# Optimization experiments

Hardware: AMD Instinct MI355X
Metric: run time of the kernel (lower is better)

Reference implementation:

```python
import jax, jax.numpy as jnp
import numpy as np
import math

# dims
B, T, D = 2, 1024, 1024
HQ, HKV, KD, VD = 16, 4, 64, 64   # query heads, kv heads, key dim, value dim
G = HQ // HKV                      # query group size
E, TOPK, CAP_FRAC, HID = 8, 2, 0.5, 2048
BASE = 10000.0
EPS = 1e-6


def setup_inputs() -> dict:
    key = jax.random.key(0)
    ks = jax.random.split(key, 12)
    s = jnp.float32(0.02)
    return {
        'x': jax.random.normal(ks[0], (B, T, D), jnp.float32),
        'wq': jax.random.normal(ks[1], (D, KD * HQ), jnp.float32) * s,
        'wk': jax.random.normal(ks[2], (D, KD * HKV), jnp.float32) * s,
        'wv': jax.random.normal(ks[3], (D, VD * HKV), jnp.float32) * s,
        'wo': jax.random.normal(ks[4], (G * HKV * VD, D), jnp.float32) * s,
        'router_w': jax.random.normal(ks[5], (D, E), jnp.float32) * s,
        'router_b': jax.random.normal(ks[6], (E,), jnp.float32) * s,
        'w1': jax.random.normal(ks[7], (E, D, HID), jnp.float32) * s,
        'w2': jax.random.normal(ks[8], (E, D, HID), jnp.float32) * s,
        'w3': jax.random.normal(ks[9], (E, HID, D), jnp.float32) * s,
        'norm1_scale': jnp.ones((D,), jnp.float32),
        'norm2_scale': jnp.ones((D,), jnp.float32),
    }


def _rms(x, scale):
    return x * jax.lax.rsqrt(jnp.mean(x * x, axis=-1, keepdims=True) + EPS) * scale


def _rope(x):
    # x: (B, t, H, d); rotary per RotaryEmbedding: tile(ticks,(1,2)), neg-half rotation
    t, d = x.shape[1], x.shape[3]
    thetas = BASE ** (-jnp.arange(0, d, 2, dtype=jnp.float32) / d)
    ticks = jnp.outer(jnp.arange(t, dtype=jnp.float32), thetas)
    ticks = jnp.tile(ticks, (1, 2))[None, :, None, :]
    cos, sin = jnp.cos(ticks).astype(x.dtype), jnp.sin(ticks).astype(x.dtype)
    x1, x2 = jnp.split(x, 2, axis=-1)
    neg = jnp.concatenate([-x2, x1], axis=-1)
    return x * cos + neg * sin


def reference(x, wq, wk, wv, wo, router_w, router_b, w1, w2, w3, norm1_scale, norm2_scale):
    b, t, d = x.shape
    # ---- pre-norm grouped-query attention with rotary, causal ----
    h = _rms(x, norm1_scale)
    q = (h @ wq).reshape(b, t, HQ, KD)
    k = (h @ wk).reshape(b, t, HKV, KD)
    v = (h @ wv).reshape(b, t, HKV, VD)
    q = _rope(q)
    k = _rope(k)
    qg = q.reshape(b, t, HKV, G, KD)
    scores = jnp.einsum('bthgk,bshk->bhgts', qg, k) / jnp.sqrt(jnp.asarray(KD, x.dtype))
    causal = jnp.tril(jnp.ones((t, t), bool))
    scores = jnp.where(causal, scores, jnp.asarray(-1e9, scores.dtype))
    probs = jax.nn.softmax(scores, axis=-1)
    attn = jnp.einsum('bhgts,bshv->bthgv', probs, v).reshape(b, t, HQ * VD)
    x = x + attn @ wo
    # ---- pre-norm top-k MoE feed-forward (capacity-masked dispatch/combine) ----
    h2 = _rms(x, norm2_scale)
    xf = h2.reshape(b * t, d)
    logits = xf.astype(jnp.float32) @ router_w + router_b        # router in fp32
    gate, assign = jax.lax.top_k(logits, TOPK)                   # (N,k)
    gate = jax.nn.softmax(gate, axis=-1).astype(x.dtype)
    cap = math.floor(b * t * CAP_FRAC)
    onehot = jax.nn.one_hot(assign, E, dtype=jnp.float32)        # (N,k,E)
    pos = jnp.cumsum(jnp.cumsum(onehot, axis=0), axis=1).astype(jnp.int32)
    mask = onehot * (pos < cap)                                  # capacity mask
    token_mask = jnp.sum(mask, axis=-1)                          # (N,k)
    choices = jnp.sum(jax.nn.one_hot(pos, cap, dtype=jnp.float32) * mask[..., None], axis=1)  # (N,E,cap)
    choices = choices.transpose(1, 2, 0)                         # (E,cap,N)
    exp_idx = jnp.einsum('tke,e->tk', mask, jnp.arange(E, dtype=jnp.float32)).astype(jnp.int32)
    pos_idx = jnp.einsum('tke,tke->tk', mask, pos.astype(jnp.float32)).astype(jnp.int32)
    grouped = jnp.einsum('ect,tD->ecD', choices.astype(x.dtype), xf)  # dispatch: (E,cap,D)
    # gated FF per expert: act(w2(x) * w1(x)) @ w3
    hh = jax.nn.gelu(jnp.einsum('ecd,edh->ech', grouped, w2) * jnp.einsum('ecd,edh->ech', grouped, w1))
    eout = jnp.einsum('ech,ehd->ecd', hh, w3)                    # (E,cap,D)
    gathered = eout[exp_idx, pos_idx].reshape(b, t, TOPK, d)
    tm = token_mask.reshape(b, t, TOPK)
    moe = jnp.where(tm[..., None] != 0, gathered, h2[:, :, None, :])  # dropped tokens fall back to input
    moe = jnp.einsum('btkD,btk->btD', moe, gate.reshape(b, t, TOPK))
    return x + moe
```

## Files before the change

### kernel.cpp

```cpp
#include <hip/hip_runtime.h>
#include <math.h>

#define Dm 1024
#define Tn 1024
#define Bn 2
#define NTOK 2048
#define HQn 16
#define HKVn 4
#define KDn 64
#define VDn 64
#define Gn 4
#define NE 8
#define CAPn 1024
#define HIDn 2048
#define QKVS 1536

using frag_ab = __attribute__((ext_vector_type(8))) short;
using f32x4  = __attribute__((ext_vector_type(4))) float;

__device__ __forceinline__ unsigned short f2bf(float f) {
    union { float f; unsigned int u; } v; v.f = f;
    unsigned int r = v.u + 0x7FFFu + ((v.u >> 16) & 1u);
    return (unsigned short)(r >> 16);
}
__device__ __forceinline__ float bf2f(unsigned short b) {
    union { unsigned int u; float f; } v; v.u = ((unsigned int)b) << 16;
    return v.f;
}
__device__ __forceinline__ float gelu_fast(float y) {
    float z = 0.7978845608028654f * (y + 0.044715f * y * y * y);
    float az = fabsf(z);
    float t = __expf(-2.f * az);
    float th = (1.f - t) / (1.f + t);
    th = copysignf(th, z);
    return 0.5f * y * (1.f + th);
}

#define GLOAD16(gp, lp) __builtin_amdgcn_global_load_lds( \
    (const __attribute__((address_space(1))) void*)(gp), \
    (__attribute__((address_space(3))) void*)(lp), 16, 0, 0)

__global__ void rmsnorm_bf16_kernel(const float* __restrict__ x, const float* __restrict__ scale,
                                    unsigned short* __restrict__ out) {
    int row = blockIdx.x;
    const float* xr = x + (size_t)row * Dm;
    float ss = 0.f;
    for (int d = threadIdx.x; d < Dm; d += 256) { float v = xr[d]; ss += v * v; }
    __shared__ float red[256];
    red[threadIdx.x] = ss; __syncthreads();
    for (int s = 128; s > 0; s >>= 1) {
        if (threadIdx.x < s) red[threadIdx.x] += red[threadIdx.x + s];
        __syncthreads();
    }
    float inv = rsqrtf(red[0] * (1.f / Dm) + 1e-6f);
    for (int d = threadIdx.x; d < Dm; d += 256)
        out[(size_t)row * Dm + d] = f2bf(xr[d] * inv * scale[d]);
}

__global__ void rmsnorm_router_kernel(const float* __restrict__ x2, const float* __restrict__ scale,
                                      const float* __restrict__ rw, const float* __restrict__ rb,
                                      float* __restrict__ h2, int* __restrict__ assign,
                                      float* __restrict__ gate) {
    int row = blockIdx.x;
    const float* xr = x2 + (size_t)row * Dm;
    __shared__ float red[256];
    __shared__ float rowbuf[Dm];
    __shared__ float logits[NE];
    float v4[4]; float ss = 0.f;
    #pragma unroll
    for (int i = 0; i < 4; ++i) { v4[i] = xr[threadIdx.x + 256 * i]; ss += v4[i] * v4[i]; }
    red[threadIdx.x] = ss; __syncthreads();
    for (int s = 128; s > 0; s >>= 1) {
        if (threadIdx.x < s) red[threadIdx.x] += red[threadIdx.x + s];
        __syncthreads();
    }
    float inv = rsqrtf(red[0] * (1.f / Dm) + 1e-6f);
    #pragma unroll
    for (int i = 0; i < 4; ++i) {
        int d = threadIdx.x + 256 * i;
        float h = v4[i] * inv * scale[d];
        h2[(size_t)row * Dm + d] = h;
        rowbuf[d] = h;
    }
    __syncthreads();
    int e = threadIdx.x >> 5, lane32 = threadIdx.x & 31;
    float part = 0.f;
    for (int d = lane32; d < Dm; d += 32) part += rowbuf[d] * rw[(size_t)d * NE + e];
    for (int off = 16; off; off >>= 1) part += __shfl_down(part, off, 32);
    if (lane32 == 0) logits[e] = part + rb[e];
    __syncthreads();
    if (threadIdx.x == 0) {
        int i0 = 0; float m0 = logits[0];
        for (int i = 1; i < NE; ++i) if (logits[i] > m0) { m0 = logits[i]; i0 = i; }
        int i1 = -1; float m1 = -1e30f;
        for (int i = 0; i < NE; ++i) if (i != i0 && logits[i] > m1) { m1 = logits[i]; i1 = i; }
        float e1 = __expf(m1 - m0);
        float s = 1.f + e1;
        assign[row * 2] = i0; assign[row * 2 + 1] = i1;
        gate[row * 2] = 1.f / s; gate[row * 2 + 1] = e1 / s;
    }
}

__global__ void transpose_convert(const float* __restrict__ in, unsigned short* __restrict__ out,
                                  int R, int Cstride, int c_base) {
    int e = blockIdx.z;
    int Cext = gridDim.x * 64;
    in  += (size_t)e * R * Cstride;
    out += (size_t)e * R * Cext;
    __shared__ float T[64][65];
    int tid = threadIdx.x;
    int r0 = blockIdx.y * 64, c0 = blockIdx.x * 64;
    #pragma unroll
    for (int rep = 0; rep < 4; ++rep) {
        int r = (tid >> 4) + rep * 16;
        int c = (tid & 15) * 4;
        float4 v = *(const float4*)(in + (size_t)(r0 + r) * Cstride + c_base + c0 + c);
        T[r][c] = v.x; T[r][c + 1] = v.y; T[r][c + 2] = v.z; T[r][c + 3] = v.w;
    }
    __syncthreads();
    #pragma unroll
    for (int rep = 0; rep < 4; ++rep) {
        int c = rep * 16 + (tid >> 4);
        int r = (tid & 15) * 4;
        unsigned long long pk = (unsigned long long)f2bf(T[r][c])
                              | ((unsigned long long)f2bf(T[r + 1][c]) << 16)
                              | ((unsigned long long)f2bf(T[r + 2][c]) << 32)
                              | ((unsigned long long)f2bf(T[r + 3][c]) << 48);
        *(unsigned long long*)(out + (size_t)(c0 + c) * R + r0 + r) = pk;
    }
}

template<int MODE>
__global__ __launch_bounds__(256) void mfma_gemm2(const unsigned short* __restrict__ A,
                                                  const unsigned short* __restrict__ Bt,
                                                  void* __restrict__ Cout,
                                                  const float* __restrict__ R,
                                                  int N, int K) {
    int m0 = blockIdx.y * 128, n0 = blockIdx.x * 128;
    __shared__ unsigned short As[128 * 32];
    __shared__ unsigned short Bs[128 * 32];
    int tid = threadIdx.x, wave = tid >> 6, lane = tid & 63;
    int quad = lane >> 4, r16 = lane & 15;
    int wm = wave & 1, wn = wave >> 1;
    int ch16 = ((lane & 3) ^ ((lane >> 3) & 3)) * 16;
    int rofs = (quad ^ ((r16 >> 1) & 3)) * 16;
    f32x4 acc[4][4];
    #pragma unroll
    for (int mt = 0; mt < 4; ++mt)
        #pragma unroll
        for (int nt = 0; nt < 4; ++nt) acc[mt][nt] = (f32x4){0.f, 0.f, 0.f, 0.f};
    const size_t rs = (size_t)K * 2;
    const char* ga0 = (const char*)A  + (size_t)m0 * rs;
    const char* gb0 = (const char*)Bt + (size_t)n0 * rs;
    for (int kk = 0; kk < K; kk += 32) {
        __syncthreads();
        #pragma unroll
        for (int i = 0; i < 2; ++i) {
            int r = wave * 16 + i * 64 + (lane >> 2);
            size_t go = (size_t)r * rs + (size_t)kk * 2 + ch16;
            int lofs = wave * 1024 + i * 4096;
            GLOAD16(ga0 + go, (char*)As + lofs);
            GLOAD16(gb0 + go, (char*)Bs + lofs);
        }
        __syncthreads();
        frag_ab a[4], b[4];
        #pragma unroll
        for (int t = 0; t < 4; ++t) {
            a[t] = *(const frag_ab*)((const char*)As + (wm * 64 + t * 16 + r16) * 64 + rofs);
            b[t] = *(const frag_ab*)((const char*)Bs + (wn * 64 + t * 16 + r16) * 64 + rofs);
        }
        #pragma unroll
        for (int mt = 0; mt < 4; ++mt)
            #pragma unroll
            for (int nt = 0; nt < 4; ++nt)
                acc[mt][nt] = __builtin_amdgcn_mfma_f32_16x16x32_bf16(a[mt], b[nt], acc[mt][nt], 0, 0, 0);
    }
    #pragma unroll
    for (int mt = 0; mt < 4; ++mt)
        #pragma unroll
        for (int nt = 0; nt < 4; ++nt)
            #pragma unroll
            for (int r = 0; r < 4; ++r) {
                int m = m0 + wm * 64 + mt * 16 + quad * 4 + r;
                int n = n0 + wn * 64 + nt * 16 + r16;
                size_t idx = (size_t)m * N + n;
                float v = acc[mt][nt][r];
                if (MODE == 0) ((unsigned short*)Cout)[idx] = f2bf(v);
                else           ((float*)Cout)[idx] = v + R[idx];
            }
}

__global__ void rope_bf16(unsigned short* __restrict__ p) {
    int idx = blockIdx.x * 256 + threadIdx.x;
    const int QC = NTOK * HQn * 32;
    int i, col, row; float scale;
    if (idx < QC) {
        i = idx & 31; int h = (idx >> 5) & 15; row = idx >> 9;
        col = h * 64 + i; scale = 0.18033688011112042f;
    } else {
        int r = idx - QC;
        i = r & 31; int h = (r >> 5) & 3; row = r >> 7;
        col = 1024 + h * 64 + i; scale = 1.f;
    }
    int t = row & (Tn - 1);
    size_t base = (size_t)row * QKVS + col;
    float theta = __expf(-(float)i * (1.f / 32.f) * 9.210340371976184f);
    float ang = (float)t * theta;
    float c = cosf(ang), s = sinf(ang);
    float x1 = bf2f(p[base]), x2 = bf2f(p[base + 32]);
    p[base]      = f2bf((x1 * c - x2 * s) * scale);
    p[base + 32] = f2bf((x2 * c + x1 * s) * scale);
}

__global__ __launch_bounds__(256) void mfma_attn(const unsigned short* __restrict__ qkv,
                                                 unsigned short* __restrict__ attnb) {
    __shared__ unsigned short lds[32768];
    unsigned short* Ps = lds;
    unsigned short* Ks = lds + 16384;
    unsigned short* Vt = lds + 24576;
    int tid = threadIdx.x, wave = tid >> 6, lane = tid & 63;
    int quad = lane >> 4, r16 = lane & 15;
    int tq0 = blockIdx.x * 128, h = blockIdx.y, b = blockIdx.z;
    int kvh = h >> 2;
    const size_t rowb = QKVS * 2;

    {
        const char* qb = (const char*)(qkv + (size_t)(b * Tn + tq0) * QKVS + h * 64);
        int rloc = lane >> 3, ch = (lane & 7) ^ rloc;
        #pragma unroll
        for (int i = 0; i < 4; ++i) {
            int r0 = wave * 8 + i * 32;
            __builtin_amdgcn_global_load_lds(
                (const __attribute__((address_space(1))) void*)(qb + (size_t)(r0 + rloc) * rowb + ch * 16),
                (__attribute__((address_space(3))) void*)((char*)Vt + r0 * 128), 16, 0, 0);
        }
    }
    __syncthreads();
    frag_ab qf[2][2];
    #pragma unroll
    for (int mt = 0; mt < 2; ++mt)
        #pragma unroll
        for (int ks = 0; ks < 2; ++ks) {
            int m = wave * 32 + mt * 16 + r16;
            int ch = (ks * 4 + quad) ^ (m & 7);
            qf[mt][ks] = *(const frag_ab*)((const char*)Vt + m * 128 + ch * 16);
        }

    float m_i[2][4], l_i[2][4];
    f32x4 O[2][4];
    #pragma unroll
    for (int mt = 0; mt < 2; ++mt) {
        #pragma unroll
        for (int r = 0; r < 4; ++r) { m_i[mt][r] = -1e30f; l_i[mt][r] = 0.f; }
        #pragma unroll
        for (int nt = 0; nt < 4; ++nt) O[mt][nt] = (f32x4){0.f, 0.f, 0.f, 0.f};
    }

    int nst = blockIdx.x + 1;
    for (int st = 0; st < nst; ++st) {
        int s0 = st * 128;
        __syncthreads();
        {
            const char* kb = (const char*)(qkv + (size_t)(b * Tn + s0) * QKVS + 1024 + kvh * 64);
            int rloc = lane >> 3, ch = (lane & 7) ^ rloc;
            #pragma unroll
            for (int i = 0; i < 4; ++i) {
                int r0 = wave * 8 + i * 32;
                __builtin_amdgcn_global_load_lds(
                    (const __attribute__((address_space(1))) void*)(kb + (size_t)(r0 + rloc) * rowb + ch * 16),
                    (__attribute__((address_space(3))) void*)((char*)Ks + r0 * 128), 16, 0, 0);
            }
        }
        {
            const unsigned short* vb = qkv + (size_t)(b * Tn + s0) * QKVS + 1280 + kvh * 64;
            int d4 = (tid & 15) * 4;
            #pragma unroll
            for (int pass = 0; pass < 4; ++pass) {
                int sl = 8 * wave + 2 * (lane >> 4) + pass * 32;
                ushort4 v0 = *(const ushort4*)(vb + (size_t)sl * QKVS + d4);
                ushort4 v1 = *(const ushort4*)(vb + (size_t)(sl + 1) * QKVS + d4);
                unsigned short a0[4] = {v0.x, v0.y, v0.z, v0.w};
                unsigned short a1[4] = {v1.x, v1.y, v1.z, v1.w};
                #pragma unroll
                for (int i = 0; i < 4; ++i) {
                    int d = d4 + i;
                    int col = (((sl >> 3) ^ (d & 15)) << 3) | (sl & 7);
                    *(unsigned int*)(Vt + d * 128 + col) =
                        (unsigned int)a0[i] | ((unsigned int)a1[i] << 16);
                }
            }
        }
        __syncthreads();
        f32x4 Sacc[2][8];
        #pragma unroll
        for (int mt = 0; mt < 2; ++mt)
            #pragma unroll
            for (int nt = 0; nt < 8; ++nt) Sacc[mt][nt] = (f32x4){0.f, 0.f, 0.f, 0.f};
        #pragma unroll
        for (int ks = 0; ks < 2; ++ks) {
            frag_ab kf[8];
            #pragma unroll
            for (int nt = 0; nt < 8; ++nt) {
                int n = nt * 16 + r16;
                int ch = (ks * 4 + quad) ^ (n & 7);
                kf[nt] = *(const frag_ab*)((const char*)Ks + n * 128 + ch * 16);
            }
            #pragma unroll
            for (int mt = 0; mt < 2; ++mt)
                #pragma unroll
                for (int nt = 0; nt < 8; ++nt)
                    Sacc[mt][nt] = __builtin_amdgcn_mfma_f32_16x16x32_bf16(qf[mt][ks], kf[nt], Sacc[mt][nt], 0, 0, 0);
        }
        if (st == nst - 1) {
            #pragma unroll
            for (int mt = 0; mt < 2; ++mt) {
                int trow = wave * 32 + mt * 16 + quad * 4;
                #pragma unroll
                for (int nt = 0; nt < 8; ++nt) {
                    int scol = nt * 16 + r16;
                    #pragma unroll
                    for (int r = 0; r < 4; ++r)
                        if (scol > trow + r) Sacc[mt][nt][r] = -1e30f;
                }
            }
        }
        #pragma unroll
        for (int mt = 0; mt < 2; ++mt) {
            float mx[4];
            #pragma unroll
            for (int r = 0; r < 4; ++r) {
                float m_ = Sacc[mt][0][r];
                #pragma unroll
                for (int nt = 1; nt < 8; ++nt) m_ = fmaxf(m_, Sacc[mt][nt][r]);
                mx[r] = m_;
            }
            #pragma unroll
            for (int off = 1; off < 16; off <<= 1)
                #pragma unroll
                for (int r = 0; r < 4; ++r) mx[r] = fmaxf(mx[r], __shfl_xor(mx[r], off));
            #pragma unroll
            for (int r = 0; r < 4; ++r) {
                float mn = fmaxf(m_i[mt][r], mx[r]);
                float al = exp2f(m_i[mt][r] - mn);
                m_i[mt][r] = mn;
                l_i[mt][r] *= al;
                #pragma unroll
                for (int nt = 0; nt < 4; ++nt) O[mt][nt][r] *= al;
            }
            float rsum[4] = {0.f, 0.f, 0.f, 0.f};
            #pragma unroll
            for (int nt = 0; nt < 8; ++nt)
                #pragma unroll
                for (int r = 0; r < 4; ++r) {
                    float pv = exp2f(Sacc[mt][nt][r] - m_i[mt][r]);
                    Sacc[mt][nt][r] = pv;
                    rsum[r] += pv;
                }
            #pragma unroll
            for (int off = 1; off < 16; off <<= 1)
                #pragma unroll
                for (int r = 0; r < 4; ++r) rsum[r] += __shfl_xor(rsum[r], off);
            #pragma unroll
            for (int r = 0; r < 4; ++r) l_i[mt][r] += rsum[r];
            #pragma unroll
            for (int nt = 0; nt < 8; ++nt) {
                int scol = nt * 16 + r16;
                int chb = scol >> 3;
                #pragma unroll
                for (int r = 0; r < 4; ++r) {
                    int m = wave * 32 + mt * 16 + quad * 4 + r;
                    int col = ((chb ^ (m & 15)) << 3) | (scol & 7);
                    Ps[m * 128 + col] = f2bf(Sacc[mt][nt][r]);
                }
            }
        }
        #pragma unroll
        for (int ks = 0; ks < 4; ++ks) {
            frag_ab pa[2], vf[4];
            #pragma unroll
            for (int mt = 0; mt < 2; ++mt) {
                int m = wave * 32 + mt * 16 + r16;
                int ch = (ks * 4 + quad) ^ (m & 15);
                pa[mt] = *(const frag_ab*)((const char*)Ps + m * 256 + ch * 16);
            }
            #pragma unroll
            for (int nt = 0; nt < 4; ++nt) {
                int n = nt * 16 + r16;
                int ch = (ks * 4 + quad) ^ (n & 15);
                vf[nt] = *(const frag_ab*)((const char*)Vt + n * 256 + ch * 16);
            }
            #pragma unroll
            for (int mt = 0; mt < 2; ++mt)
                #pragma unroll
                for (int nt = 0; nt < 4; ++nt)
                    O[mt][nt] = __builtin_amdgcn_mfma_f32_16x16x32_bf16(pa[mt], vf[nt], O[mt][nt], 0, 0, 0);
        }
    }
    #pragma unroll
    for (int mt = 0; mt < 2; ++mt) {
        float inv[4];
        #pragma unroll
        for (int r = 0; r < 4; ++r) inv[r] = 1.f / l_i[mt][r];
        #pragma unroll
        for (int nt = 0; nt < 4; ++nt)
            #pragma unroll
            for (int r = 0; r < 4; ++r) {
                int t = tq0 + wave * 32 + mt * 16 + quad * 4 + r;
                int c = h * 64 + nt * 16 + r16;
                attnb[(size_t)(b * Tn + t) * Dm + c] = f2bf(O[mt][nt][r] * inv[r]);
            }
    }
}

__global__ void scan_kernel(const int* __restrict__ assign, int* __restrict__ pos,
                            int* __restrict__ limit) {
    __shared__ int cnt[256][16];
    __shared__ int tot[16];
    int tid = threadIdx.x;
    int local[16];
    #pragma unroll
    for (int i = 0; i < 16; ++i) local[i] = 0;
    for (int r = 0; r < 8; ++r) {
        int t = tid * 8 + r;
        local[assign[t * 2]]++;
        local[8 + assign[t * 2 + 1]]++;
    }
    #pragma unroll
    for (int i = 0; i < 16; ++i) cnt[tid][i] = local[i];
    __syncthreads();
    if (tid < 16) {
        int run = 0;
        for (int th = 0; th < 256; ++th) { int v = cnt[th][tid]; cnt[th][tid] = run; run += v; }
        tot[tid] = run;
    }
    __syncthreads();
    int r0[NE], r1[NE];
    #pragma unroll
    for (int e = 0; e < NE; ++e) { r0[e] = cnt[tid][e]; r1[e] = cnt[tid][8 + e]; }
    for (int r = 0; r < 8; ++r) {
        int t = tid * 8 + r;
        int e0 = assign[t * 2], e1 = assign[t * 2 + 1];
        r0[e0]++; pos[t * 2] = r0[e0];
        r1[e1]++; pos[t * 2 + 1] = r0[e1] + r1[e1];
    }
    if (tid == 0)
        for (int e = 0; e < NE; ++e) {
            int C = tot[e] + tot[8 + e];
            limit[e] = C < (CAPn - 1) ? C : (CAPn - 1);
        }
}

__global__ void dispatch_kernel(const float* __restrict__ h2, const int* __restrict__ assign,
                                const int* __restrict__ pos, float* __restrict__ grouped) {
    int slot = blockIdx.x;
    int p = pos[slot];
    if (p >= CAPn) return;
    int e = assign[slot];
    const float* src = h2 + (size_t)(slot >> 1) * Dm;
    float* dst = grouped + ((size_t)e * CAPn + p) * Dm;
    for (int d = threadIdx.x; d < Dm; d += 256) atomicAdd(&dst[d], src[d]);
}

__global__ void convert_inplace(float* __restrict__ buf) {
    float* rp = buf + (size_t)blockIdx.x * Dm;
    float4 v = ((const float4*)rp)[threadIdx.x];
    __syncthreads();
    unsigned long long pk = (unsigned long long)f2bf(v.x)
                          | ((unsigned long long)f2bf(v.y) << 16)
                          | ((unsigned long long)f2bf(v.z) << 32)
                          | ((unsigned long long)f2bf(v.w) << 48);
    ((unsigned long long*)rp)[threadIdx.x] = pk;
}

__global__ __launch_bounds__(256) void mfma_gemm_fused(const float* __restrict__ grouped,
                                                       const unsigned short* __restrict__ B1t,
                                                       const unsigned short* __restrict__ B2t,
                                                       unsigned short* __restrict__ hh,
                                                       const int* __restrict__ limit) {
    int e = blockIdx.z;
    int m0 = blockIdx.y * 128;
    if (m0 > limit[e]) return;
    int n0 = blockIdx.x * 128;
    const char* ga0 = (const char*)grouped + ((size_t)e * CAPn + m0) * 4096;
    const unsigned short* b1 = B1t + (size_t)e * 1024 * Dm;
    const unsigned short* b2 = B2t + (size_t)e * 1024 * Dm;
    unsigned short* Ch = hh + (size_t)e * CAPn * 1024;
    __shared__ unsigned short As[128 * 32];
    __shared__ unsigned short Bs[128 * 32];
    int tid = threadIdx.x, wave = tid >> 6, lane = tid & 63;
    int quad = lane >> 4, r16 = lane & 15;
    int wm = wave & 1, wn = wave >> 1;
    int ch16 = ((lane & 3) ^ ((lane >> 3) & 3)) * 16;
    int rofs = (quad ^ ((r16 >> 1) & 3)) * 16;
    f32x4 acc[4][4];
    #pragma unroll
    for (int mt = 0; mt < 4; ++mt)
        #pragma unroll
        for (int nt = 0; nt < 4; ++nt) acc[mt][nt] = (f32x4){0.f, 0.f, 0.f, 0.f};
    for (int kk = 0; kk < Dm; kk += 32) {
        __syncthreads();
        #pragma unroll
        for (int i = 0; i < 2; ++i) {
            int r = wave * 16 + i * 64 + (lane >> 2);
            int lofs = wave * 1024 + i * 4096;
            GLOAD16(ga0 + (size_t)r * 4096 + (size_t)kk * 2 + ch16, (char*)As + lofs);
            const unsigned short* bb = (r & 1) ? b2 : b1;
            size_t go = (size_t)((n0 + r) >> 1) * 2048 + (size_t)kk * 2 + ch16;
            GLOAD16((const char*)bb + go, (char*)Bs + lofs);
        }
        __syncthreads();
        frag_ab a[4], b[4];
        #pragma unroll
        for (int t = 0; t < 4; ++t) {
            a[t] = *(const frag_ab*)((const char*)As + (wm * 64 + t * 16 + r16) * 64 + rofs);
            b[t] = *(const frag_ab*)((const char*)Bs + (wn * 64 + t * 16 + r16) * 64 + rofs);
        }
        #pragma unroll
        for (int mt = 0; mt < 4; ++mt)
            #pragma unroll
            for (int nt = 0; nt < 4; ++nt)
                acc[mt][nt] = __builtin_amdgcn_mfma_f32_16x16x32_bf16(a[mt], b[nt], acc[mt][nt], 0, 0, 0);
    }
    #pragma unroll
    for (int mt = 0; mt < 4; ++mt)
        #pragma unroll
        for (int nt = 0; nt < 4; ++nt)
            #pragma unroll
            for (int r = 0; r < 4; ++r) {
                float v = acc[mt][nt][r];
                float w = __shfl_xor(v, 1);
                if (!(r16 & 1)) {
                    int m = m0 + wm * 64 + mt * 16 + quad * 4 + r;
                    int j = (n0 + wn * 64 + nt * 16 + r16) >> 1;
                    Ch[(size_t)m * 1024 + j] = f2bf(gelu_fast(v * w));
                }
            }
}

__global__ __launch_bounds__(256) void mfma_gemm_w3(const unsigned short* __restrict__ hhA,
                                                    const unsigned short* __restrict__ hhB,
                                                    const unsigned short* __restrict__ Bt,
                                                    unsigned short* __restrict__ C,
                                                    const int* __restrict__ limit) {
    int e = blockIdx.z;
    int m0 = blockIdx.y * 128;
    if (m0 > limit[e]) return;
    int n0 = blockIdx.x * 64;
    const char* gaA = (const char*)hhA + ((size_t)e * CAPn + m0) * 2048;
    const char* gaB = (const char*)hhB + ((size_t)e * CAPn + m0) * 2048;
    const char* gb0 = (const char*)Bt + ((size_t)e * 1024 + n0) * 4096;
    C += (size_t)e * CAPn * 1024;
    __shared__ unsigned short As[128 * 32];
    __shared__ unsigned short Bs[64 * 32];
    int tid = threadIdx.x, wave = tid >> 6, lane = tid & 63;
    int quad = lane >> 4, r16 = lane & 15;
    int wm = wave & 1, wn = wave >> 1;
    int ch16 = ((lane & 3) ^ ((lane >> 3) & 3)) * 16;
    int rofs = (quad ^ ((r16 >> 1) & 3)) * 16;
    f32x4 acc[4][2];
    #pragma unroll
    for (int mt = 0; mt < 4; ++mt)
        #pragma unroll
        for (int nt = 0; nt < 2; ++nt) acc[mt][nt] = (f32x4){0.f, 0.f, 0.f, 0.f};
    for (int kk = 0; kk < HIDn; kk += 32) {
        const char* ga = (kk < 1024) ? gaA : gaB;
        size_t kb = (size_t)(kk & 1023) * 2;
        __syncthreads();
        #pragma unroll
        for (int i = 0; i < 2; ++i) {
            int r = wave * 16 + i * 64 + (lane >> 2);
            GLOAD16(ga + (size_t)r * 2048 + kb + ch16, (char*)As + wave * 1024 + i * 4096);
        }
        {
            int r = wave * 16 + (lane >> 2);
            GLOAD16(gb0 + (size_t)r * 4096 + (size_t)kk * 2 + ch16, (char*)Bs + wave * 1024);
        }
        __syncthreads();
        frag_ab a[4], b[2];
        #pragma unroll
        for (int t = 0; t < 4; ++t)
            a[t] = *(const frag_ab*)((const char*)As + (wm * 64 + t * 16 + r16) * 64 + rofs);
        #pragma unroll
        for (int t = 0; t < 2; ++t)
            b[t] = *(const frag_ab*)((const char*)Bs + (wn * 32 + t * 16 + r16) * 64 + rofs);
        #pragma unroll
        for (int mt = 0; mt < 4; ++mt)
            #pragma unroll
            for (int nt = 0; nt < 2; ++nt)
                acc[mt][nt] = __builtin_amdgcn_mfma_f32_16x16x32_bf16(a[mt], b[nt], acc[mt][nt], 0, 0, 0);
    }
    #pragma unroll
    for (int mt = 0; mt < 4; ++mt)
        #pragma unroll
        for (int nt = 0; nt < 2; ++nt)
            #pragma unroll
            for (int r = 0; r < 4; ++r) {
                int m = m0 + wm * 64 + mt * 16 + quad * 4 + r;
                int n = n0 + wn * 32 + nt * 16 + r16;
                C[(size_t)m * 1024 + n] = f2bf(acc[mt][nt][r]);
            }
}

__global__ void combine_kernel(const float* __restrict__ x2, const float* __restrict__ h2,
                               const unsigned short* __restrict__ eout, const int* __restrict__ assign,
                               const int* __restrict__ pos, const float* __restrict__ gate,
                               float* __restrict__ out) {
    int t = blockIdx.x;
    int e0 = assign[t * 2], e1 = assign[t * 2 + 1];
    int p0 = pos[t * 2],   p1 = pos[t * 2 + 1];
    float g0 = gate[t * 2], g1 = gate[t * 2 + 1];
    bool k0 = p0 < CAPn, k1 = p1 < CAPn;
    const unsigned short* s0 = eout + ((size_t)e0 * CAPn + p0) * Dm;
    const unsigned short* s1 = eout + ((size_t)e1 * CAPn + p1) * Dm;
    const float* hb = h2 + (size_t)t * Dm;
    for (int d = threadIdx.x; d < Dm; d += 256) {
        float v0 = k0 ? bf2f(s0[d]) : hb[d];
        float v1 = k1 ? bf2f(s1[d]) : hb[d];
        out[(size_t)t * Dm + d] = x2[(size_t)t * Dm + d] + g0 * v0 + g1 * v1;
    }
}

extern "C" void kernel_launch(void* const* d_in, const int* in_sizes, int n_in,
                              void* d_out, int out_size, void* d_ws, size_t ws_size,
                              hipStream_t stream) {
    const float* x        = (const float*)d_in[0];
    const float* wq       = (const float*)d_in[1];
    const float* wk       = (const float*)d_in[2];
    const float* wv       = (const float*)d_in[3];
    const float* wo       = (const float*)d_in[4];
    const float* router_w = (const float*)d_in[5];
    const float* router_b = (const float*)d_in[6];
    const float* w1       = (const float*)d_in[7];
    const float* w2       = (const float*)d_in[8];
    const float* w3       = (const float*)d_in[9];
    const float* n1s      = (const float*)d_in[10];
    const float* n2s      = (const float*)d_in[11];
    float* out = (float*)d_out;
    unsigned char* ws = (unsigned char*)d_ws;
    const size_t MB = 1ull << 20;

    unsigned short* h_bf  = (unsigned short*)(ws + 0 * MB);
    unsigned short* qkv   = (unsigned short*)(ws + 4 * MB);
    unsigned short* wqkvt = (unsigned short*)(ws + 10 * MB);
    unsigned short* attnb = (unsigned short*)(ws + 13 * MB);
    unsigned short* wot   = (unsigned short*)(ws + 17 * MB);
    float* grouped_f32    = (float*)(ws + 0 * MB);
    unsigned short* eout  = (unsigned short*)(ws + 0 * MB);
    float* x2      = (float*)(ws + 32 * MB);
    float* h2      = (float*)(ws + 40 * MB);
    int*   assign  = (int*)  (ws + 48 * MB);
    int*   pos     = (int*)  (ws + 48 * MB + 65536);
    float* gate    = (float*)(ws + 48 * MB + 131072);
    int*   limit   = (int*)  (ws + 48 * MB + 196608);
    unsigned short* wtA = (unsigned short*)(ws + 49 * MB);
    unsigned short* wtB = (unsigned short*)(ws + 65 * MB);
    unsigned short* wt3 = (unsigned short*)(ws + 49 * MB);
    unsigned short* hhA = (unsigned short*)(ws + 81 * MB);
    unsigned short* hhB = (unsigned short*)(ws + 97 * MB);
    (void)in_sizes; (void)n_in; (void)out_size; (void)ws_size;

    transpose_convert<<<dim3(16, 16, 1), 256, 0, stream>>>(wq, wqkvt, Dm, Dm, 0);
    transpose_convert<<<dim3(4, 16, 1), 256, 0, stream>>>(wk, wqkvt + 1024 * 1024, Dm, 256, 0);
    transpose_convert<<<dim3(4, 16, 1), 256, 0, stream>>>(wv, wqkvt + 1280 * 1024, Dm, 256, 0);
    transpose_convert<<<dim3(16, 16, 1), 256, 0, stream>>>(wo, wot, Dm, Dm, 0);
    rmsnorm_bf16_kernel<<<NTOK, 256, 0, stream>>>(x, n1s, h_bf);
    mfma_gemm2<0><<<dim3(QKVS / 128, NTOK / 128), 256, 0, stream>>>(h_bf, wqkvt, qkv, nullptr, QKVS, Dm);
    rope_bf16<<<(NTOK * (HQn + HKVn) * 32) / 256, 256, 0, stream>>>(qkv);
    mfma_attn<<<dim3(Tn / 128, HQn, Bn), 256, 0, stream>>>(qkv, attnb);
    mfma_gemm2<1><<<dim3(Dm / 128, NTOK / 128), 256, 0, stream>>>(attnb, wot, x2, x, Dm, Dm);
    rmsnorm_router_kernel<<<NTOK, 256, 0, stream>>>(x2, n2s, router_w, router_b, h2, assign, gate);
    scan_kernel<<<1, 256, 0, stream>>>(assign, pos, limit);
    hipMemsetAsync(grouped_f32, 0, (size_t)NE * CAPn * Dm * sizeof(float), stream);
    dispatch_kernel<<<NTOK * 2, 256, 0, stream>>>(h2, assign, pos, grouped_f32);
    convert_inplace<<<NE * CAPn, 256, 0, stream>>>(grouped_f32);
    transpose_convert<<<dim3(16, 16, NE), 256, 0, stream>>>(w1, wtA, Dm, HIDn, 0);
    transpose_convert<<<dim3(16, 16, NE), 256, 0, stream>>>(w2, wtB, Dm, HIDn, 0);
    mfma_gemm_fused<<<dim3(16, CAPn / 128, NE), 256, 0, stream>>>(grouped_f32, wtA, wtB, hhA, limit);
    transpose_convert<<<dim3(16, 16, NE), 256, 0, stream>>>(w1, wtA, Dm, HIDn, 1024);
    transpose_convert<<<dim3(16, 16, NE), 256, 0, stream>>>(w2, wtB, Dm, HIDn, 1024);
    mfma_gemm_fused<<<dim3(16, CAPn / 128, NE), 256, 0, stream>>>(grouped_f32, wtA, wtB, hhB, limit);
    transpose_convert<<<dim3(16, 32, NE), 256, 0, stream>>>(w3, wt3, HIDn, Dm, 0);
    mfma_gemm_w3<<<dim3(16, CAPn / 128, NE), 256, 0, stream>>>(hhA, hhB, wt3, eout, limit);
    combine_kernel<<<NTOK, 256, 0, stream>>>(x2, h2, eout, assign, pos, gate, out);
}
```

Before: 561.5 us.

## Triple-buffer LDS loads in MFMA GEMMs and swizzle workgroup order across XCDs

Rewrites the GEMM main loops (QKV/output projection, fused w1/w2, and w3) to prefetch two K-steps ahead into a 3-stage LDS ring buffer. Per-step syncs become explicit vmcnt waits plus raw barriers, so global-to-LDS loads can overlap MFMA work. The grids are also flattened to 1D with a swizzle that maps consecutive blocks to the same XCD-strided tile groups, aiming for better L2 locality. This triples LDS use per block, which may reduce occupancy, and the hand-counted vmcnt values must match the number of loads issued per stage.

```diff
diff --git a/kernel.cpp b/kernel.cpp
--- a/kernel.cpp
+++ b/kernel.cpp
@@ -39,6 +39,11 @@
 #define GLOAD16(gp, lp) __builtin_amdgcn_global_load_lds( \
     (const __attribute__((address_space(1))) void*)(gp), \
     (__attribute__((address_space(3))) void*)(lp), 16, 0, 0)
+
+#define LGKM_DRAIN() do { \
+    asm volatile("s_waitcnt lgkmcnt(0)" ::: "memory"); \
+    __builtin_amdgcn_sched_barrier(0); \
+} while (0)
 
 __global__ void rmsnorm_bf16_kernel(const float* __restrict__ x, const float* __restrict__ scale,
                                     unsigned short* __restrict__ out) {
@@ -135,10 +140,13 @@
                                                   const unsigned short* __restrict__ Bt,
                                                   void* __restrict__ Cout,
                                                   const float* __restrict__ R,
-                                                  int N, int K) {
-    int m0 = blockIdx.y * 128, n0 = blockIdx.x * 128;
-    __shared__ unsigned short As[128 * 32];
-    __shared__ unsigned short Bs[128 * 32];
+                                                  int N, int K, int nx) {
+    int nwg = gridDim.x;
+    int swz = (blockIdx.x & 7) * (nwg >> 3) + (blockIdx.x >> 3);
+    int bx = swz % nx, by = swz / nx;
+    int m0 = by * 128, n0 = bx * 128;
+    __shared__ unsigned short As[3][128 * 32];
+    __shared__ unsigned short Bs[3][128 * 32];
     int tid = threadIdx.x, wave = tid >> 6, lane = tid & 63;
     int quad = lane >> 4, r16 = lane & 15;
     int wm = wave & 1, wn = wave >> 1;
@@ -152,28 +160,48 @@
     const size_t rs = (size_t)K * 2;
     const char* ga0 = (const char*)A  + (size_t)m0 * rs;
     const char* gb0 = (const char*)Bt + (size_t)n0 * rs;
-    for (int kk = 0; kk < K; kk += 32) {
-        __syncthreads();
+    auto stage = [&](int buf, int kk) {
         #pragma unroll
         for (int i = 0; i < 2; ++i) {
             int r = wave * 16 + i * 64 + (lane >> 2);
             size_t go = (size_t)r * rs + (size_t)kk * 2 + ch16;
             int lofs = wave * 1024 + i * 4096;
-            GLOAD16(ga0 + go, (char*)As + lofs);
-            GLOAD16(gb0 + go, (char*)Bs + lofs);
-        }
-        __syncthreads();
+            GLOAD16(ga0 + go, (char*)As[buf] + lofs);
+            GLOAD16(gb0 + go, (char*)Bs[buf] + lofs);
+        }
+    };
+    int nsteps = K >> 5;
+    stage(0, 0);
+    if (nsteps > 1) stage(1, 32);
+    int rd = 0, stg = 2;
+    for (int t = 0; t < nsteps; ++t) {
+        if (t) __builtin_amdgcn_s_barrier();
+        if (t + 2 < nsteps) {
+            stage(stg, (t + 2) << 5);
+            stg = (stg == 2) ? 0 : stg + 1;
+            asm volatile("s_waitcnt vmcnt(8)" ::: "memory");
+        } else if (t + 1 < nsteps) {
+            asm volatile("s_waitcnt vmcnt(4)" ::: "memory");
+        } else {
+            asm volatile("s_waitcnt vmcnt(0)" ::: "memory");
+        }
+        __builtin_amdgcn_s_barrier();
+        asm volatile("" ::: "memory");
+        const char* Ab = (const char*)As[rd];
+        const char* Bb = (const char*)Bs[rd];
+        rd = (rd == 2) ? 0 : rd + 1;
         frag_ab a[4], b[4];
         #pragma unroll
-        for (int t = 0; t < 4; ++t) {
-            a[t] = *(const frag_ab*)((const char*)As + (wm * 64 + t * 16 + r16) * 64 + rofs);
-            b[t] = *(const frag_ab*)((const char*)Bs + (wn * 64 + t * 16 + r16) * 64 + rofs);
+        for (int tt = 0; tt < 4; ++tt) {
+            a[tt] = *(const frag_ab*)(Ab + (wm * 64 + tt * 16 + r16) * 64 + rofs);
+            b[tt] = *(const frag_ab*)(Bb + (wn * 64 + tt * 16 + r16) * 64 + rofs);
         }
         #pragma unroll
         for (int mt = 0; mt < 4; ++mt)
             #pragma unroll
             for (int nt = 0; nt < 4; ++nt)
                 acc[mt][nt] = __builtin_amdgcn_mfma_f32_16x16x32_bf16(a[mt], b[nt], acc[mt][nt], 0, 0, 0);
+        LGKM_DRAIN();
     }
     #pragma unroll
     for (int mt = 0; mt < 4; ++mt)
@@ -477,16 +505,18 @@
                                                        const unsigned short* __restrict__ B2t,
                                                        unsigned short* __restrict__ hh,
                                                        const int* __restrict__ limit) {
-    int e = blockIdx.z;
-    int m0 = blockIdx.y * 128;
+    int lin = blockIdx.x;
+    int swz = (lin & 7) * (gridDim.x >> 3) + (lin >> 3);
+    int e = swz >> 7;
+    int m0 = ((swz >> 4) & 7) * 128;
     if (m0 > limit[e]) return;
-    int n0 = blockIdx.x * 128;
+    int n0 = (swz & 15) * 128;
     const char* ga0 = (const char*)grouped + ((size_t)e * CAPn + m0) * 4096;
     const unsigned short* b1 = B1t + (size_t)e * 1024 * Dm;
     const unsigned short* b2 = B2t + (size_t)e * 1024 * Dm;
     unsigned short* Ch = hh + (size_t)e * CAPn * 1024;
-    __shared__ unsigned short As[128 * 32];
-    __shared__ unsigned short Bs[128 * 32];
+    __shared__ unsigned short As[3][128 * 32];
+    __shared__ unsigned short Bs[3][128 * 32];
     int tid = threadIdx.x, wave = tid >> 6, lane = tid & 63;
     int quad = lane >> 4, r16 = lane & 15;
     int wm = wave & 1, wn = wave >> 1;
@@ -497,29 +527,49 @@
     for (int mt = 0; mt < 4; ++mt)
         #pragma unroll
         for (int nt = 0; nt < 4; ++nt) acc[mt][nt] = (f32x4){0.f, 0.f, 0.f, 0.f};
-    for (int kk = 0; kk < Dm; kk += 32) {
-        __syncthreads();
+    auto stage = [&](int buf, int kk) {
         #pragma unroll
         for (int i = 0; i < 2; ++i) {
             int r = wave * 16 + i * 64 + (lane >> 2);
             int lofs = wave * 1024 + i * 4096;
-            GLOAD16(ga0 + (size_t)r * 4096 + (size_t)kk * 2 + ch16, (char*)As + lofs);
+            GLOAD16(ga0 + (size_t)r * 4096 + (size_t)kk * 2 + ch16, (char*)As[buf] + lofs);
             const unsigned short* bb = (r & 1) ? b2 : b1;
             size_t go = (size_t)((n0 + r) >> 1) * 2048 + (size_t)kk * 2 + ch16;
-            GLOAD16((const char*)bb + go, (char*)Bs + lofs);
-        }
-        __syncthreads();
+            GLOAD16((const char*)bb + go, (char*)Bs[buf] + lofs);
+        }
+    };
+    const int nsteps = Dm >> 5;
+    stage(0, 0);
+    stage(1, 32);
+    int rd = 0, stg = 2;
+    for (int t = 0; t < nsteps; ++t) {
+        if (t) __builtin_amdgcn_s_barrier();
+        if (t + 2 < nsteps) {
+            stage(stg, (t + 2) << 5);
+            stg = (stg == 2) ? 0 : stg + 1;
+            asm volatile("s_waitcnt vmcnt(8)" ::: "memory");
+        } else if (t + 1 < nsteps) {
+            asm volatile("s_waitcnt vmcnt(4)" ::: "memory");
+        } else {
+            asm volatile("s_waitcnt vmcnt(0)" ::: "memory");
+        }
+        __builtin_amdgcn_s_barrier();
+        asm volatile("" ::: "memory");
+        const char* Ab = (const char*)As[rd];
+        const char* Bb = (const char*)Bs[rd];
+        rd = (rd == 2) ? 0 : rd + 1;
         frag_ab a[4], b[4];
         #pragma unroll
-        for (int t = 0; t < 4; ++t) {
-            a[t] = *(const frag_ab*)((const char*)As + (wm * 64 + t * 16 + r16) * 64 + rofs);
-            b[t] = *(const frag_ab*)((const char*)Bs + (wn * 64 + t * 16 + r16) * 64 + rofs);
+        for (int tt = 0; tt < 4; ++tt) {
+            a[tt] = *(const frag_ab*)(Ab + (wm * 64 + tt * 16 + r16) * 64 + rofs);
+            b[tt] = *(const frag_ab*)(Bb + (wn * 64 + tt * 16 + r16) * 64 + rofs);
         }
         #pragma unroll
         for (int mt = 0; mt < 4; ++mt)
             #pragma unroll
             for (int nt = 0; nt < 4; ++nt)
                 acc[mt][nt] = __builtin_amdgcn_mfma_f32_16x16x32_bf16(a[mt], b[nt], acc[mt][nt], 0, 0, 0);
+        LGKM_DRAIN();
     }
     #pragma unroll
     for (int mt = 0; mt < 4; ++mt)
@@ -542,16 +592,18 @@
                                                     const unsigned short* __restrict__ Bt,
                                                     unsigned short* __restrict__ C,
                                                     const int* __restrict__ limit) {
-    int e = blockIdx.z;
-    int m0 = blockIdx.y * 128;
+    int lin = blockIdx.x;
+    int swz = (lin & 7) * (gridDim.x >> 3) + (lin >> 3);
+    int e = swz >> 7;
+    int m0 = ((swz >> 4) & 7) * 128;
     if (m0 > limit[e]) return;
-    int n0 = blockIdx.x * 64;
+    int n0 = (swz & 15) * 64;
     const char* gaA = (const char*)hhA + ((size_t)e * CAPn + m0) * 2048;
     const char* gaB = (const char*)hhB + ((size_t)e * CAPn + m0) * 2048;
     const char* gb0 = (const char*)Bt + ((size_t)e * 1024 + n0) * 4096;
     C += (size_t)e * CAPn * 1024;
-    __shared__ unsigned short As[128 * 32];
-    __shared__ unsigned short Bs[64 * 32];
+    __shared__ unsigned short As[3][128 * 32];
+    __shared__ unsigned short Bs[3][64 * 32];
     int tid = threadIdx.x, wave = tid >> 6, lane = tid & 63;
     int quad = lane >> 4, r16 = lane & 15;
     int wm = wave & 1, wn = wave >> 1;
@@ -562,32 +614,50 @@
     for (int mt = 0; mt < 4; ++mt)
         #pragma unroll
         for (int nt = 0; nt < 2; ++nt) acc[mt][nt] = (f32x4){0.f, 0.f, 0.f, 0.f};
-    for (int kk = 0; kk < HIDn; kk += 32) {
+    auto stage = [&](int buf, int kk) {
         const char* ga = (kk < 1024) ? gaA : gaB;
         size_t kb = (size_t)(kk & 1023) * 2;
-        __syncthreads();
         #pragma unroll
         for (int i = 0; i < 2; ++i) {
             int r = wave * 16 + i * 64 + (lane >> 2);
-            GLOAD16(ga + (size_t)r * 2048 + kb + ch16, (char*)As + wave * 1024 + i * 4096);
-        }
-        {
-            int r = wave * 16 + (lane >> 2);
-            GLOAD16(gb0 + (size_t)r * 4096 + (size_t)kk * 2 + ch16, (char*)Bs + wave * 1024);
-        }
-        __syncthreads();
+            GLOAD16(ga + (size_t)r * 2048 + kb + ch16, (char*)As[buf] + wave * 1024 + i * 4096);
+        }
+        int r = wave * 16 + (lane >> 2);
+        GLOAD16(gb0 + (size_t)r * 4096 + (size_t)kk * 2 + ch16, (char*)Bs[buf] + wave * 1024);
+    };
+    const int nsteps = HIDn >> 5;
+    stage(0, 0);
+    stage(1, 32);
+    int rd = 0, stg = 2;
+    for (int t = 0; t < nsteps; ++t) {
+        if (t) __builtin_amdgcn_s_barrier();
+        if (t + 2 < nsteps) {
+            stage(stg, (t + 2) << 5);
+            stg = (stg == 2) ? 0 : stg + 1;
+            asm volatile("s_waitcnt vmcnt(6)" ::: "memory");
+        } else if (t + 1 < nsteps) {
+            asm volatile("s_waitcnt vmcnt(3)" ::: "memory");
+        } else {
+            asm volatile("s_waitcnt vmcnt(0)" ::: "memory");
+        }
+        __builtin_amdgcn_s_barrier();
+        asm volatile("" ::: "memory");
+        const char* Ab = (const char*)As[rd];
+        const char* Bb = (const char*)Bs[rd];
+        rd = (rd == 2) ? 0 : rd + 1;
         frag_ab a[4], b[2];
         #pragma unroll
-        for (int t = 0; t < 4; ++t)
-            a[t] = *(const frag_ab*)((const char*)As + (wm * 64 + t * 16 + r16) * 64 + rofs);
-        #pragma unroll
-        for (int t = 0; t < 2; ++t)
-            b[t] = *(const frag_ab*)((const char*)Bs + (wn * 32 + t * 16 + r16) * 64 + rofs);
+        for (int tt = 0; tt < 4; ++tt)
+            a[tt] = *(const frag_ab*)(Ab + (wm * 64 + tt * 16 + r16) * 64 + rofs);
+        #pragma unroll
+        for (int tt = 0; tt < 2; ++tt)
+            b[tt] = *(const frag_ab*)(Bb + (wn * 32 + tt * 16 + r16) * 64 + rofs);
         #pragma unroll
         for (int mt = 0; mt < 4; ++mt)
             #pragma unroll
             for (int nt = 0; nt < 2; ++nt)
                 acc[mt][nt] = __builtin_amdgcn_mfma_f32_16x16x32_bf16(a[mt], b[nt], acc[mt][nt], 0, 0, 0);
+        LGKM_DRAIN();
     }
     #pragma unroll
     for (int mt = 0; mt < 4; ++mt)
@@ -664,10 +734,10 @@
     transpose_convert<<<dim3(4, 16, 1), 256, 0, stream>>>(wv, wqkvt + 1280 * 1024, Dm, 256, 0);
     transpose_convert<<<dim3(16, 16, 1), 256, 0, stream>>>(wo, wot, Dm, Dm, 0);
     rmsnorm_bf16_kernel<<<NTOK, 256, 0, stream>>>(x, n1s, h_bf);
-    mfma_gemm2<0><<<dim3(QKVS / 128, NTOK / 128), 256, 0, stream>>>(h_bf, wqkvt, qkv, nullptr, QKVS, Dm);
+    mfma_gemm2<0><<<dim3((QKVS / 128) * (NTOK / 128)), 256, 0, stream>>>(h_bf, wqkvt, qkv, nullptr, QKVS, Dm, QKVS / 128);
     rope_bf16<<<(NTOK * (HQn + HKVn) * 32) / 256, 256, 0, stream>>>(qkv);
     mfma_attn<<<dim3(Tn / 128, HQn, Bn), 256, 0, stream>>>(qkv, attnb);
-    mfma_gemm2<1><<<dim3(Dm / 128, NTOK / 128), 256, 0, stream>>>(attnb, wot, x2, x, Dm, Dm);
+    mfma_gemm2<1><<<dim3((Dm / 128) * (NTOK / 128)), 256, 0, stream>>>(attnb, wot, x2, x, Dm, Dm, Dm / 128);
     rmsnorm_router_kernel<<<NTOK, 256, 0, stream>>>(x2, n2s, router_w, router_b, h2, assign, gate);
     scan_kernel<<<1, 256, 0, stream>>>(assign, pos, limit);
     hipMemsetAsync(grouped_f32, 0, (size_t)NE * CAPn * Dm * sizeof(float), stream);
@@ -675,11 +745,11 @@
     convert_inplace<<<NE * CAPn, 256, 0, stream>>>(grouped_f32);
     transpose_convert<<<dim3(16, 16, NE), 256, 0, stream>>>(w1, wtA, Dm, HIDn, 0);
     transpose_convert<<<dim3(16, 16, NE), 256, 0, stream>>>(w2, wtB, Dm, HIDn, 0);
-    mfma_gemm_fused<<<dim3(16, CAPn / 128, NE), 256, 0, stream>>>(grouped_f32, wtA, wtB, hhA, limit);
+    mfma_gemm_fused<<<dim3(16 * (CAPn / 128) * NE), 256, 0, stream>>>(grouped_f32, wtA, wtB, hhA, limit);
     transpose_convert<<<dim3(16, 16, NE), 256, 0, stream>>>(w1, wtA, Dm, HIDn, 1024);
     transpose_convert<<<dim3(16, 16, NE), 256, 0, stream>>>(w2, wtB, Dm, HIDn, 1024);
-    mfma_gemm_fused<<<dim3(16, CAPn / 128, NE), 256, 0, stream>>>(grouped_f32, wtA, wtB, hhB, limit);
+    mfma_gemm_fused<<<dim3(16 * (CAPn / 128) * NE), 256, 0, stream>>>(grouped_f32, wtA, wtB, hhB, limit);
     transpose_convert<<<dim3(16, 32, NE), 256, 0, stream>>>(w3, wt3, HIDn, Dm, 0);
-    mfma_gemm_w3<<<dim3(16, CAPn / 128, NE), 256, 0, stream>>>(hhA, hhB, wt3, eout, limit);
+    mfma_gemm_w3<<<dim3(16 * (CAPn / 128) * NE), 256, 0, stream>>>(hhA, hhB, wt3, eout, limit);
     combine_kernel<<<NTOK, 256, 0, stream>>>(x2, h2, eout, assign, pos, gate, out);
 }
```

After: 551.5 us. No clear change (-1.8%).
